# Performance work log

Measured on AMD Instinct MI355X. Metric: run time of the kernel, lower is better.

## Reference

```python
import math
import jax, jax.numpy as jnp
import numpy as np

RANK = 8
OUT_H, OUT_W = 512, 512
CTX = 512
EPS = 1e-12          # module eps (fp32 path)
NORM_EPS = 1e-12     # torch F.normalize default eps
REPULSION = 0.1
NOISE = 0.01
OUT_FEATS = 26 * RANK + 2  # 24r + 2r + 2


def _l2norm(x):
    n = jnp.sqrt(jnp.sum(x * x, axis=-1, keepdims=True))
    return x / jnp.maximum(n, NORM_EPS)


def _stable(x):
    # forward: clamp tiny magnitudes to +/-eps; backward: identity (straight-through)
    s = jnp.where(jnp.abs(x) < EPS, jnp.sign(x) * EPS, x)
    return x + jax.lax.stop_gradient(s - x)


def setup_inputs() -> dict:
    key = jax.random.key(0)
    k1, k2, k3, k4 = jax.random.split(key, 4)
    x = jax.random.normal(k1, (4, CTX), jnp.float32)
    # xavier_uniform for Linear(CTX -> OUT_FEATS)
    bound = math.sqrt(6.0 / (CTX + OUT_FEATS))
    ctx_w = jax.random.uniform(k2, (OUT_FEATS, CTX), jnp.float32, -bound, bound)
    ctx_b = jax.random.uniform(k3, (OUT_FEATS,), jnp.float32, -1.0, 1.0) / math.sqrt(CTX)
    weights = jax.random.normal(k4, (1, RANK, 2, 2, OUT_H, OUT_W, 2), jnp.float32) * 1e-5
    return {"x": x, "ctx_w": ctx_w, "ctx_b": ctx_b, "weights": weights}


def reference(x, ctx_w, ctx_b, weights):
    r = RANK
    B = x.shape[0]
    xt = x @ ctx_w.T + ctx_b                      # [B, 26r+2]
    sa = 13 * r + 1                               # slice_attention
    xt = xt[:, :sa] * jnp.tanh(xt[:, sa:])        # [B, 13r+1]
    mod = xt[:, : 12 * r].reshape(B, r, 3, 2, 1, 1, 2)  # [B,r,3,2,1,1,2]
    shift_lerp = jnp.array([0.5, 0.0], xt.dtype)
    shift_scale = jnp.array([1.0, 0.0], xt.dtype)
    c = mod[:, :, 0] + shift_lerp                 # [B,r,2,1,1,2]
    bias = mod[:, :, 1]
    scale = mod[:, :, 2] + shift_scale
    w0, w1 = weights[:, :, 0], weights[:, :, 1]   # [1,r,2,H,W,2]
    # complex lerp: z = w0 + c*(w1 - w0)
    dr = w1[..., 0] - w0[..., 0]
    di = w1[..., 1] - w0[..., 1]
    lr = w0[..., 0] + c[..., 0] * dr - c[..., 1] * di
    li = w0[..., 1] + c[..., 0] * di + c[..., 1] * dr
    # complex addmul: z = bias + z*scale
    zr = bias[..., 0] + lr * scale[..., 0] - li * scale[..., 1]
    zi = bias[..., 1] + lr * scale[..., 1] + li * scale[..., 0]
    z = jnp.stack([zr, zi], axis=-1)              # [B,r,2,H,W,2]
    num, den = z[:, :, 0], z[:, :, 1]             # [B,r,H,W,2]
    dnorm = jnp.sqrt(jnp.clip(jnp.sum(den * den, -1), EPS, None))[..., None]
    theta = den / dnorm
    w = jnp.sum(num * theta, -1)                  # [B,r,H,W]
    wf = w.reshape(B, r, -1)                      # [B,r,H*W]
    wf = _l2norm(_stable(wf))
    # self-similarity repulsion (small r x r matmuls)
    sim = jnp.einsum('brn,bsn->brs', wf, wf)
    sim = sim * (1.0 - jnp.eye(r, dtype=wf.dtype))
    rep = jnp.einsum('brs,bsn->brn', sim, wf) / (r - 1)
    wf = wf - rep * (REPULSION / math.sqrt(r))
    wf = _l2norm(_stable(wf))
    # deterministic noise injection (training mode with fixed key)
    mean = jax.lax.stop_gradient(jnp.mean(wf, -1, keepdims=True))
    std = jax.lax.stop_gradient(jnp.clip(jnp.std(wf, -1, keepdims=True, ddof=1), EPS, None))
    noise = jax.random.normal(jax.random.key(42), wf.shape, wf.dtype)
    wf = wf + jax.lax.stop_gradient((noise * std + mean) * NOISE)
    w = wf.reshape(B, r, OUT_H, OUT_W)
    w = jnp.concatenate([w, jnp.zeros((B, 1, OUT_H, OUT_W), w.dtype)], axis=1)  # drain
    wr = xt[:, 12 * r:]                           # [B, r+1]
    wr = jnp.concatenate([wr[:, :-1], wr[:, -1:] + 1.0 / math.sqrt(r)], axis=-1)
    wr = jax.nn.softmax(_l2norm(wr), axis=-1)
    return jnp.sum(w * wr[:, :, None, None], axis=1)  # [B,H,W]
```

## Files before the change

### kernel.cpp

```cpp
#include <hip/hip_runtime.h>
#include <math.h>

#define NPIX 262144
#define BATCH 4
#define RANK 8
#define CTXD 512
#define OUTF 210

#define XT_OFF   0
#define ACC_OFF  1024
#define REP      8
#define NACC     176
#define WFS_OFF  4096
#define ZERO_BYTE (ACC_OFF * 4)
#define ZERO_LEN  (REP * NACC * 4)

__device__ __forceinline__ float dpp_sum64(float x) {
  x += __int_as_float(__builtin_amdgcn_update_dpp(0, __float_as_int(x), 0x111, 0xf, 0xf, true));
  x += __int_as_float(__builtin_amdgcn_update_dpp(0, __float_as_int(x), 0x112, 0xf, 0xf, true));
  x += __int_as_float(__builtin_amdgcn_update_dpp(0, __float_as_int(x), 0x114, 0xf, 0xf, true));
  x += __int_as_float(__builtin_amdgcn_update_dpp(0, __float_as_int(x), 0x118, 0xf, 0xf, true));
  x += __int_as_float(__builtin_amdgcn_update_dpp(0, __float_as_int(x), 0x142, 0xf, 0xf, true));
  x += __int_as_float(__builtin_amdgcn_update_dpp(0, __float_as_int(x), 0x143, 0xf, 0xf, true));
  return x;
}

__device__ __forceinline__ void threefry2x32_pair(unsigned int x0, unsigned int x1,
                                                  unsigned int* o0, unsigned int* o1) {
  const unsigned int ks0 = 0u, ks1 = 42u, ks2 = 0x1BD11BF0u;
  x0 += ks0; x1 += ks1;
#define TF_R(rot) { x0 += x1; x1 = (x1 << rot) | (x1 >> (32 - rot)); x1 ^= x0; }
  TF_R(13) TF_R(15) TF_R(26) TF_R(6)
  x0 += ks1; x1 += ks2 + 1u;
  TF_R(17) TF_R(29) TF_R(16) TF_R(24)
  x0 += ks2; x1 += ks0 + 2u;
  TF_R(13) TF_R(15) TF_R(26) TF_R(6)
  x0 += ks0; x1 += ks1 + 3u;
  TF_R(17) TF_R(29) TF_R(16) TF_R(24)
  x0 += ks1; x1 += ks2 + 4u;
  TF_R(13) TF_R(15) TF_R(26) TF_R(6)
  x0 += ks2; x1 += ks0 + 5u;
#undef TF_R
  *o0 = x0; *o1 = x1;
}

__device__ __forceinline__ float fast_normal(unsigned int bits) {
  unsigned int fb = (bits >> 9) | 0x3f800000u;
  float f = __uint_as_float(fb) - 1.0f;
  const float lo = -0.99999994039535522461f;
  float u = f * 2.0f + lo;
  u = fmaxf(u, lo);
  float w = -__logf(fmaf(-u, u, 1.0f));
  float q1 = w - 2.5f;
  float p1 = 2.81022636e-08f;
  p1 = fmaf(p1, q1, 3.43273939e-07f);
  p1 = fmaf(p1, q1, -3.5233877e-06f);
  p1 = fmaf(p1, q1, -4.39150654e-06f);
  p1 = fmaf(p1, q1, 0.00021858087f);
  p1 = fmaf(p1, q1, -0.00125372503f);
  p1 = fmaf(p1, q1, -0.00417768164f);
  p1 = fmaf(p1, q1, 0.246640727f);
  p1 = fmaf(p1, q1, 1.50140941f);
  float q2 = sqrtf(w) - 3.0f;
  float p2 = -0.000200214257f;
  p2 = fmaf(p2, q2, 0.000100950558f);
  p2 = fmaf(p2, q2, 0.00134934322f);
  p2 = fmaf(p2, q2, -0.00367342844f);
  p2 = fmaf(p2, q2, 0.00573950773f);
  p2 = fmaf(p2, q2, -0.0076224613f);
  p2 = fmaf(p2, q2, 0.00943887047f);
  p2 = fmaf(p2, q2, 1.00167406f);
  p2 = fmaf(p2, q2, 2.83297682f);
  float pr = (w < 5.0f) ? p1 : p2;
  return 1.4142135623730951f * pr * u;
}

__global__ __launch_bounds__(256) void k_ctx(const float* __restrict__ x,
                                             const float* __restrict__ cw,
                                             const float* __restrict__ cb,
                                             float* __restrict__ ws) {
  int lane = threadIdx.x & 63, wv = threadIdx.x >> 6;
  int row = blockIdx.x * 4 + wv;
  int b = row / OUTF, i = row - b * OUTF;
  const float* wrow = cw + i * CTXD;
  const float* xr = x + b * CTXD;
  float acc = 0.f;
#pragma unroll
  for (int u = 0; u < CTXD; u += 64)
    acc = fmaf(wrow[u + lane], xr[u + lane], acc);
  acc = dpp_sum64(acc);
  if (lane == 63) ws[XT_OFF + row] = acc + cb[i];
}

__global__ __launch_bounds__(256) void k_wfs(const float* __restrict__ wts,
                                             float* __restrict__ ws) {
  __shared__ float gl[BATCH * 96];
  __shared__ float gred[4][NACC];
  const float* xt = ws + XT_OFF;
  float* wfs = ws + WFS_OFF;
  int t = threadIdx.x;
  for (int i = t; i < BATCH * 96; i += 256) {
    int b = i / 96, j = i - b * 96;
    gl[i] = xt[b * OUTF + j] * tanhf(xt[b * OUTF + 105 + j]);
  }
  __syncthreads();

  int p = blockIdx.x * 256 + t;
  const float2* w2 = (const float2*)wts;
  float wf[BATCH][RANK];
#pragma unroll
  for (int k = 0; k < RANK; ++k) {
    float2 W0c0 = w2[((k * 4 + 0) << 18) + p];
    float2 W0c1 = w2[((k * 4 + 1) << 18) + p];
    float2 W1c0 = w2[((k * 4 + 2) << 18) + p];
    float2 W1c1 = w2[((k * 4 + 3) << 18) + p];
#pragma unroll
    for (int b = 0; b < BATCH; ++b) {
      const float* gb = gl + b * 96 + 12 * k;
      float zr0, zi0, zr1, zi1;
      {
        float c0 = gb[0] + 0.5f, c1 = gb[1], b0 = gb[4], b1 = gb[5];
        float s0 = gb[8] + 1.0f, s1 = gb[9];
        float dr = W1c0.x - W0c0.x, di = W1c0.y - W0c0.y;
        float lr = W0c0.x + c0 * dr - c1 * di;
        float li = W0c0.y + c0 * di + c1 * dr;
        zr0 = b0 + lr * s0 - li * s1;
        zi0 = b1 + lr * s1 + li * s0;
      }
      {
        float c0 = gb[2] + 0.5f, c1 = gb[3], b0 = gb[6], b1 = gb[7];
        float s0 = gb[10] + 1.0f, s1 = gb[11];
        float dr = W1c1.x - W0c1.x, di = W1c1.y - W0c1.y;
        float lr = W0c1.x + c0 * dr - c1 * di;
        float li = W0c1.y + c0 * di + c1 * dr;
        zr1 = b0 + lr * s0 - li * s1;
        zi1 = b1 + lr * s1 + li * s0;
      }
      float d2 = zr1 * zr1 + zi1 * zi1;
      float dn = sqrtf(fmaxf(d2, 1e-12f));
      float w = (zr0 * zr1 + zi0 * zi1) / dn;
      if (fabsf(w) < 1e-12f) w = (w > 0.f) ? 1e-12f : ((w < 0.f) ? -1e-12f : 0.f);
      wf[b][k] = w;
      wfs[((b * RANK + k) << 18) + p] = w;
    }
  }
  int lane = t & 63, wv = t >> 6;
#pragma unroll
  for (int b = 0; b < BATCH; ++b) {
    int idx = b * 36;
#pragma unroll
    for (int r = 0; r < RANK; ++r)
#pragma unroll
      for (int s = r; s < RANK; ++s, ++idx) {
        float pr = dpp_sum64(wf[b][r] * wf[b][s]);
        if (lane == 63) gred[wv][idx] = pr;
      }
  }
#pragma unroll
  for (int b = 0; b < BATCH; ++b)
#pragma unroll
    for (int k = 0; k < RANK; ++k) {
      float pr = dpp_sum64(wf[b][k]);
      if (lane == 63) gred[wv][144 + b * 8 + k] = pr;
    }
  __syncthreads();
  if (t < NACC) {
    float s = gred[0][t] + gred[1][t] + gred[2][t] + gred[3][t];
    atomicAdd(ws + ACC_OFF + (blockIdx.x & (REP - 1)) * NACC + t, s);
  }
}

__global__ __launch_bounds__(256) void k_out(const float* __restrict__ ws,
                                             float* __restrict__ out) {
  const float* xt = ws + XT_OFF;
  const float* wfs = ws + WFS_OFF;
  __shared__ float G[NACC];
  __shared__ float n1[32], Ml[256], vv[32], scl[32], ca[4], wrl[BATCH][9];
  __shared__ float in2[32], mnv[32], sdv[32];
  int t = threadIdx.x;
  if (t < NACC) {
    float s = 0.f;
#pragma unroll
    for (int rep = 0; rep < REP; ++rep) s += ws[ACC_OFF + rep * NACC + t];
    G[t] = s;
  }
  if (t >= 192 && t < 192 + BATCH) {
    int b = t - 192;
    float raw[9];
#pragma unroll
    for (int j = 0; j < 9; ++j)
      raw[j] = xt[b * OUTF + 96 + j] * tanhf(xt[b * OUTF + 201 + j]);
    raw[8] += 0.35355339059327373f;
    double ss = 0.0;
    for (int j = 0; j < 9; ++j) ss += (double)raw[j] * (double)raw[j];
    float n = fmaxf((float)sqrt(ss), 1e-12f);
    float y[9]; float m = -1e30f;
    for (int j = 0; j < 9; ++j) { y[j] = raw[j] / n; m = fmaxf(m, y[j]); }
    float e[9]; double se = 0.0;
    for (int j = 0; j < 9; ++j) { e[j] = expf(y[j] - m); se += (double)e[j]; }
    for (int j = 0; j < 9; ++j) wrl[b][j] = e[j] / (float)se;
  }
  __syncthreads();
  if (t < 32) {
    int b = t >> 3, k = t & 7;
    int di = k * 8 - (k * (k - 1)) / 2;
    n1[t] = fmaxf(sqrtf(G[b * 36 + di]), 1e-12f);
  }
  __syncthreads();
  {
    int b = t >> 6, k = (t >> 3) & 7, s = t & 7;
    float m;
    if (k == s) {
      m = 1.0f / n1[b * 8 + k];
    } else {
      int r0 = k < s ? k : s, s0 = k < s ? s : k;
      int gi = r0 * 8 - (r0 * (r0 - 1)) / 2 + (s0 - r0);
      float simv = G[b * 36 + gi] / (n1[b * 8 + k] * n1[b * 8 + s]);
      m = -0.0050507627227610544f * simv / n1[b * 8 + s];
    }
    Ml[t] = m;
  }
  __syncthreads();
  if (t < 32) {
    int b = t >> 3, k = t & 7;
    float sum = 0.f, sq = 0.f;
#pragma unroll
    for (int s = 0; s < 8; ++s) {
      float ms = Ml[b * 64 + k * 8 + s];
      sum = fmaf(ms, G[144 + b * 8 + s], sum);
#pragma unroll
      for (int u = 0; u < 8; ++u) {
        int r0 = s < u ? s : u, s0 = s < u ? u : s;
        int gi = r0 * 8 - (r0 * (r0 - 1)) / 2 + (s0 - r0);
        sq = fmaf(ms * Ml[b * 64 + k * 8 + u], G[b * 36 + gi], sq);
      }
    }
    float n2 = fmaxf(sqrtf(fmaxf(sq, 0.f)), 1e-12f);
    float mean = sum / n2 * (1.0f / NPIX);
    float sy2 = sq / (n2 * n2);
    float var = (sy2 - (float)NPIX * mean * mean) * (1.0f / (float)(NPIX - 1));
    var = fmaxf(var, 0.f);
    float sd = fmaxf(sqrtf(var), 1e-12f);
    in2[t] = 1.f / n2; mnv[t] = mean; sdv[t] = sd;
  }
  __syncthreads();
  if (t < 32) {
    int b = t >> 3, s = t & 7;
    float acc = 0.f;
#pragma unroll
    for (int k = 0; k < 8; ++k)
      acc += wrl[b][k] * Ml[b * 64 + k * 8 + s] * in2[b * 8 + k];
    vv[t] = acc;
    scl[t] = wrl[b][s] * 0.01f * sdv[t];
  }
  if (t < BATCH) {
    float a = 0.f;
#pragma unroll
    for (int k = 0; k < 8; ++k) a += wrl[t][k] * 0.01f * mnv[t * 8 + k];
    ca[t] = a;
  }
  __syncthreads();

  int p = blockIdx.x * 256 + t;
  float o[4];
#pragma unroll
  for (int b = 0; b < 4; ++b) {
    float acc = ca[b];
#pragma unroll
    for (int s = 0; s < 8; ++s)
      acc = fmaf(vv[b * 8 + s], wfs[((b * RANK + s) << 18) + p], acc);
    o[b] = acc;
  }
#pragma unroll
  for (int bk = 0; bk < 16; ++bk) {
    unsigned int i = ((unsigned int)bk << 18) + (unsigned int)p;
    unsigned int r0, r1;
    threefry2x32_pair(i, i + 0x400000u, &r0, &r1);
    int b2 = bk >> 3, k = bk & 7;
    o[b2]     += scl[b2 * 8 + k]       * fast_normal(r0);
    o[b2 + 2] += scl[(b2 + 2) * 8 + k] * fast_normal(r1);
  }
#pragma unroll
  for (int b = 0; b < 4; ++b) out[(b << 18) + p] = o[b];
}

extern "C" void kernel_launch(void* const* d_in, const int* in_sizes, int n_in,
                              void* d_out, int out_size, void* d_ws, size_t ws_size,
                              hipStream_t stream) {
  const float* x   = (const float*)d_in[0];
  const float* cw  = (const float*)d_in[1];
  const float* cb  = (const float*)d_in[2];
  const float* wts = (const float*)d_in[3];
  float* out = (float*)d_out;
  float* ws  = (float*)d_ws;

  hipMemsetAsync((char*)d_ws + ZERO_BYTE, 0, ZERO_LEN, stream);

  k_ctx <<<210,  256, 0, stream>>>(x, cw, cb, ws);
  k_wfs <<<1024, 256, 0, stream>>>(wts, ws);
  k_out <<<1024, 256, 0, stream>>>(ws, out);
}
```

Measured before the change: 150.1 us.

## Store intermediate per-pixel weights as packed fp16 in pixel-major layout

The per-rank, per-batch intermediate values written by k_wfs are now stored as fp16, packed as 32 halves per pixel, and k_out reads them with float4 loads. k_wfs now processes two pixels per thread using float4 weight loads at 128 threads per block. This halves the intermediate buffer traffic between the two kernels. The cost is fp16 rounding of the intermediate values, which could affect accuracy.

```diff
diff --git a/kernel.cpp b/kernel.cpp
--- a/kernel.cpp
+++ b/kernel.cpp
@@ -1,4 +1,5 @@
 #include <hip/hip_runtime.h>
+#include <hip/hip_fp16.h>
 #include <math.h>
 
 #define NPIX 262144
@@ -92,57 +93,78 @@
   if (lane == 63) ws[XT_OFF + row] = acc + cb[i];
 }
 
-__global__ __launch_bounds__(256) void k_wfs(const float* __restrict__ wts,
+__global__ __launch_bounds__(128) void k_wfs(const float* __restrict__ wts,
                                              float* __restrict__ ws) {
   __shared__ float gl[BATCH * 96];
-  __shared__ float gred[4][NACC];
+  __shared__ float gred[2][NACC];
   const float* xt = ws + XT_OFF;
-  float* wfs = ws + WFS_OFF;
+  __half* wfs16 = (__half*)((char*)ws + WFS_OFF * 4);
   int t = threadIdx.x;
-  for (int i = t; i < BATCH * 96; i += 256) {
+  for (int i = t; i < BATCH * 96; i += 128) {
     int b = i / 96, j = i - b * 96;
     gl[i] = xt[b * OUTF + j] * tanhf(xt[b * OUTF + 105 + j]);
   }
   __syncthreads();
 
-  int p = blockIdx.x * 256 + t;
-  const float2* w2 = (const float2*)wts;
-  float wf[BATCH][RANK];
+  int tp = blockIdx.x * 128 + t;
+  int p0 = tp << 1;
+  const float4* w4 = (const float4*)wts;
+  float wf[BATCH][RANK][2];
 #pragma unroll
   for (int k = 0; k < RANK; ++k) {
-    float2 W0c0 = w2[((k * 4 + 0) << 18) + p];
-    float2 W0c1 = w2[((k * 4 + 1) << 18) + p];
-    float2 W1c0 = w2[((k * 4 + 2) << 18) + p];
-    float2 W1c1 = w2[((k * 4 + 3) << 18) + p];
+    float4 ld[2][2];
+#pragma unroll
+    for (int s = 0; s < 2; ++s)
+#pragma unroll
+      for (int comp = 0; comp < 2; ++comp)
+        ld[s][comp] = w4[((k * 4 + s * 2 + comp) << 17) + tp];
 #pragma unroll
     for (int b = 0; b < BATCH; ++b) {
       const float* gb = gl + b * 96 + 12 * k;
-      float zr0, zi0, zr1, zi1;
-      {
-        float c0 = gb[0] + 0.5f, c1 = gb[1], b0 = gb[4], b1 = gb[5];
-        float s0 = gb[8] + 1.0f, s1 = gb[9];
-        float dr = W1c0.x - W0c0.x, di = W1c0.y - W0c0.y;
-        float lr = W0c0.x + c0 * dr - c1 * di;
-        float li = W0c0.y + c0 * di + c1 * dr;
-        zr0 = b0 + lr * s0 - li * s1;
-        zi0 = b1 + lr * s1 + li * s0;
+      float zr[2][2], zi[2][2];
+#pragma unroll
+      for (int comp = 0; comp < 2; ++comp) {
+        float c0 = gb[2 * comp] + 0.5f;
+        float c1 = gb[2 * comp + 1];
+        float b0 = gb[4 + 2 * comp];
+        float b1 = gb[5 + 2 * comp];
+        float s0 = gb[8 + 2 * comp] + 1.0f;
+        float s1 = gb[9 + 2 * comp];
+        float4 W0 = ld[0][comp], W1 = ld[1][comp];
+#pragma unroll
+        for (int j = 0; j < 2; ++j) {
+          float w0r = j ? W0.z : W0.x;
+          float w0i = j ? W0.w : W0.y;
+          float w1r = j ? W1.z : W1.x;
+          float w1i = j ? W1.w : W1.y;
+          float dr = w1r - w0r, di = w1i - w0i;
+          float lr = w0r + c0 * dr - c1 * di;
+          float li = w0i + c0 * di + c1 * dr;
+          zr[comp][j] = b0 + lr * s0 - li * s1;
+          zi[comp][j] = b1 + lr * s1 + li * s0;
+        }
       }
-      {
-        float c0 = gb[2] + 0.5f, c1 = gb[3], b0 = gb[6], b1 = gb[7];
-        float s0 = gb[10] + 1.0f, s1 = gb[11];
-        float dr = W1c1.x - W0c1.x, di = W1c1.y - W0c1.y;
-        float lr = W0c1.x + c0 * dr - c1 * di;
-        float li = W0c1.y + c0 * di + c1 * dr;
-        zr1 = b0 + lr * s0 - li * s1;
-        zi1 = b1 + lr * s1 + li * s0;
+#pragma unroll
+      for (int j = 0; j < 2; ++j) {
+        float d2 = zr[1][j] * zr[1][j] + zi[1][j] * zi[1][j];
+        float dn = sqrtf(fmaxf(d2, 1e-12f));
+        float w = (zr[0][j] * zr[1][j] + zi[0][j] * zi[1][j]) / dn;
+        if (fabsf(w) < 1e-12f) w = (w > 0.f) ? 1e-12f : ((w < 0.f) ? -1e-12f : 0.f);
+        wf[b][k][j] = w;
       }
-      float d2 = zr1 * zr1 + zi1 * zi1;
-      float dn = sqrtf(fmaxf(d2, 1e-12f));
-      float w = (zr0 * zr1 + zi0 * zi1) / dn;
-      if (fabsf(w) < 1e-12f) w = (w > 0.f) ? 1e-12f : ((w < 0.f) ? -1e-12f : 0.f);
-      wf[b][k] = w;
-      wfs[((b * RANK + k) << 18) + p] = w;
     }
+  }
+#pragma unroll
+  for (int j = 0; j < 2; ++j) {
+    union { __half h[32]; float4 f4[4]; } pk;
+#pragma unroll
+    for (int b = 0; b < BATCH; ++b)
+#pragma unroll
+      for (int k = 0; k < RANK; ++k)
+        pk.h[b * 8 + k] = __float2half(wf[b][k][j]);
+    float4* wp = (float4*)(wfs16 + (size_t)(p0 + j) * 32);
+#pragma unroll
+    for (int i = 0; i < 4; ++i) wp[i] = pk.f4[i];
   }
   int lane = t & 63, wv = t >> 6;
 #pragma unroll
@@ -152,7 +174,7 @@
     for (int r = 0; r < RANK; ++r)
 #pragma unroll
       for (int s = r; s < RANK; ++s, ++idx) {
-        float pr = dpp_sum64(wf[b][r] * wf[b][s]);
+        float pr = dpp_sum64(wf[b][r][0] * wf[b][s][0] + wf[b][r][1] * wf[b][s][1]);
         if (lane == 63) gred[wv][idx] = pr;
       }
   }
@@ -160,20 +182,20 @@
   for (int b = 0; b < BATCH; ++b)
 #pragma unroll
     for (int k = 0; k < RANK; ++k) {
-      float pr = dpp_sum64(wf[b][k]);
+      float pr = dpp_sum64(wf[b][k][0] + wf[b][k][1]);
       if (lane == 63) gred[wv][144 + b * 8 + k] = pr;
     }
   __syncthreads();
-  if (t < NACC) {
-    float s = gred[0][t] + gred[1][t] + gred[2][t] + gred[3][t];
-    atomicAdd(ws + ACC_OFF + (blockIdx.x & (REP - 1)) * NACC + t, s);
+  for (int i = t; i < NACC; i += 128) {
+    float s = gred[0][i] + gred[1][i];
+    atomicAdd(ws + ACC_OFF + (blockIdx.x & (REP - 1)) * NACC + i, s);
   }
 }
 
 __global__ __launch_bounds__(256) void k_out(const float* __restrict__ ws,
                                              float* __restrict__ out) {
   const float* xt = ws + XT_OFF;
-  const float* wfs = ws + WFS_OFF;
+  const __half* wfs16 = (const __half*)((const char*)ws + WFS_OFF * 4);
   __shared__ float G[NACC];
   __shared__ float n1[32], Ml[256], vv[32], scl[32], ca[4], wrl[BATCH][9];
   __shared__ float in2[32], mnv[32], sdv[32];
@@ -262,13 +284,19 @@
   __syncthreads();
 
   int p = blockIdx.x * 256 + t;
+  union { __half h[32]; float4 f4[4]; } pk;
+  {
+    const float4* rp = (const float4*)(wfs16 + (size_t)p * 32);
+#pragma unroll
+    for (int i = 0; i < 4; ++i) pk.f4[i] = rp[i];
+  }
   float o[4];
 #pragma unroll
   for (int b = 0; b < 4; ++b) {
     float acc = ca[b];
 #pragma unroll
     for (int s = 0; s < 8; ++s)
-      acc = fmaf(vv[b * 8 + s], wfs[((b * RANK + s) << 18) + p], acc);
+      acc = fmaf(vv[b * 8 + s], __half2float(pk.h[b * 8 + s]), acc);
     o[b] = acc;
   }
 #pragma unroll
@@ -297,6 +325,6 @@
   hipMemsetAsync((char*)d_ws + ZERO_BYTE, 0, ZERO_LEN, stream);
 
   k_ctx <<<210,  256, 0, stream>>>(x, cw, cb, ws);
-  k_wfs <<<1024, 256, 0, stream>>>(wts, ws);
+  k_wfs <<<1024, 128, 0, stream>>>(wts, ws);
   k_out <<<1024, 256, 0, stream>>>(ws, out);
 }
```

New measurement: 305.4 us. +103.5%, slower.
